# Performance work log

Measured on AMD Instinct MI355X. Metric: run time of the kernel, lower is better.

## Reference

```python
import jax, jax.numpy as jnp
import numpy as np

B, D, R, E, L = 16384, 1024, 64, 4, 3  # batch, in_features, low_rank, expert_num, layer_num


def setup_inputs() -> dict:
    key = jax.random.key(0)
    k0, k1, k2, k3, k4 = jax.random.split(key, 5)
    x = jax.random.normal(k0, (B, D), dtype=jnp.float32)
    # xavier_normal-ish init scales
    su = (2.0 / (D + R)) ** 0.5
    sc = (2.0 / (R + R)) ** 0.5
    U = jax.random.normal(k1, (L, E, D, R), dtype=jnp.float32) * su
    V = jax.random.normal(k2, (L, E, R, D), dtype=jnp.float32) * su
    C = jax.random.normal(k3, (L, E, R, R), dtype=jnp.float32) * sc
    bias = jnp.zeros((L, D), dtype=jnp.float32)  # original (L, D, 1) squeezed
    gates_w = jax.random.normal(k4, (E, D), dtype=jnp.float32) * (1.0 / D ** 0.5)
    return {"x": x, "U": U, "V": V, "C": C, "bias": bias, "gates_w": gates_w}


def reference(x, U, V, C, bias, gates_w):
    x0 = x                                  # [B, D]
    xl = x
    n_layers = U.shape[0]
    for i in range(n_layers):               # small fixed layer count
        g = jax.nn.softmax(xl @ gates_w.T, axis=1)          # [B, E] softmax over experts
        t = jnp.tanh(jnp.einsum('erd,bd->ber', V[i], xl))   # [B, E, R]
        t = jnp.tanh(jnp.einsum('ers,bes->ber', C[i], t))   # [B, E, R]
        t = jnp.einsum('edr,ber->bed', U[i], t) + bias[i][None, None, :]  # [B, E, D]
        t = x0[:, None, :] * t                               # x0 * E_i(xl)
        xl = jnp.einsum('bed,be->bd', t, g) + xl             # gated combine + residual
    return xl
```

## Files before the change

kernel.cpp:

```cpp
#include <hip/hip_runtime.h>
#include <hip/hip_bf16.h>


using bf16x8 = __attribute__((ext_vector_type(8))) short;
using f32x4  = __attribute__((ext_vector_type(4))) float;

__device__ __forceinline__ unsigned short f2bf(float f) {
  union { __hip_bfloat16 h; unsigned short s; } u;
  u.h = __float2bfloat16(f);
  return u.s;
}
__device__ __forceinline__ unsigned int pk2(float a, float b) {
  return (unsigned int)f2bf(a) | ((unsigned int)f2bf(b) << 16);
}
__device__ __forceinline__ float fast_tanh(float x) {
  float cx = fminf(15.0f, fmaxf(-15.0f, x));
  float t = exp2f(cx * 2.885390081777927f);
  return (t - 1.0f) / (t + 1.0f);
}

__global__ void preconvert_k(const float* __restrict__ U, const float* __restrict__ V,
                             const float* __restrict__ C, const float* __restrict__ G,
                             unsigned short* __restrict__ Vb, unsigned short* __restrict__ Ub,
                             unsigned short* __restrict__ Cb, unsigned short* __restrict__ Gb) {
  int i = blockIdx.x * 256 + threadIdx.x;
  if (i < 786432) { Vb[i] = f2bf(V[i]); Ub[i] = f2bf(U[i]); }
  if (i < 49152)  Cb[i] = f2bf(C[i]);
  if (i < 4096)   Gb[i] = f2bf(G[i]);
}

__global__ __launch_bounds__(512, 2)
void crossmix_layer(const float* xl_in, float* xl_out, const float* x0,
                    const unsigned short* __restrict__ Vb,
                    const unsigned short* __restrict__ Ub,
                    const unsigned short* __restrict__ Cb,
                    const unsigned short* __restrict__ Gb,
                    const float* __restrict__ bias) {
  constexpr int BM = 64, DD = 1024, BK = 128;
  __shared__ unsigned short xlbuf[2][BM * BK];
  __shared__ unsigned short tbuf[BM * 256];
  __shared__ float g_lds[BM][4];

  const int tid  = threadIdx.x;
  const int lane = tid & 63;
  const int wave = tid >> 6;
  const int l15  = lane & 15;
  const int l4   = lane >> 4;
  const int rowbase = blockIdx.x * BM;

  float4 sv[4];
  auto stage_load = [&](int c) {
    int r = tid >> 3, cb = (tid & 7) * 16;
    const float* s = xl_in + (size_t)(rowbase + r) * DD + c * BK + cb;
    sv[0] = *(const float4*)(s);
    sv[1] = *(const float4*)(s + 4);
    sv[2] = *(const float4*)(s + 8);
    sv[3] = *(const float4*)(s + 12);
  };
  auto stage_write = [&](int buf) {
    int r = tid >> 3, cb = (tid & 7) * 16;
    uint4 p0 = make_uint4(pk2(sv[0].x, sv[0].y), pk2(sv[0].z, sv[0].w),
                          pk2(sv[1].x, sv[1].y), pk2(sv[1].z, sv[1].w));
    uint4 p1 = make_uint4(pk2(sv[2].x, sv[2].y), pk2(sv[2].z, sv[2].w),
                          pk2(sv[3].x, sv[3].y), pk2(sv[3].z, sv[3].w));
    char* lb = (char*)xlbuf[buf];
    int base = r * 256 + cb * 2;
    int swz  = (r & 7) << 4;
    *(uint4*)(lb + ((base)      ^ swz)) = p0;
    *(uint4*)(lb + ((base + 16) ^ swz)) = p1;
  };

  f32x4 zf = {0.f, 0.f, 0.f, 0.f};
  f32x4 acc1[4][2], accg[4];
  #pragma unroll
  for (int m = 0; m < 4; ++m) { acc1[m][0] = zf; acc1[m][1] = zf; accg[m] = zf; }
  const int ncol = wave * 32;

  stage_load(0); stage_write(0);
  __syncthreads();
  for (int c = 0; c < 8; ++c) {
    if (c < 7) stage_load(c + 1);
    const char* lb = (const char*)xlbuf[c & 1];
    #pragma unroll
    for (int ki = 0; ki < 4; ++ki) {
      bf16x8 afr[4];
      #pragma unroll
      for (int mt = 0; mt < 4; ++mt) {
        int row = mt * 16 + l15;
        afr[mt] = *(const bf16x8*)(lb + ((row * 256 + ki * 64 + l4 * 16) ^ ((row & 7) << 4)));
      }
      int kg = c * 128 + ki * 32 + l4 * 8;
      #pragma unroll
      for (int nt = 0; nt < 2; ++nt) {
        bf16x8 bfr = *(const bf16x8*)(Vb + (ncol + nt * 16 + l15) * 1024 + kg);
        #pragma unroll
        for (int mt = 0; mt < 4; ++mt)
          acc1[mt][nt] = __builtin_amdgcn_mfma_f32_16x16x32_bf16(afr[mt], bfr, acc1[mt][nt], 0, 0, 0);
      }
      if (wave == 0) {
        bf16x8 gfr = {0, 0, 0, 0, 0, 0, 0, 0};
        if (l15 < 4) gfr = *(const bf16x8*)(Gb + l15 * 1024 + kg);
        #pragma unroll
        for (int mt = 0; mt < 4; ++mt)
          accg[mt] = __builtin_amdgcn_mfma_f32_16x16x32_bf16(afr[mt], gfr, accg[mt], 0, 0, 0);
      }
    }
    if (c < 7) stage_write((c + 1) & 1);
    __syncthreads();
  }

  if (wave == 0 && l15 < 4) {
    #pragma unroll
    for (int mt = 0; mt < 4; ++mt)
      #pragma unroll
      for (int rg = 0; rg < 4; ++rg)
        g_lds[mt * 16 + l4 * 4 + rg][l15] = accg[mt][rg];
  }
  #pragma unroll
  for (int mt = 0; mt < 4; ++mt)
    #pragma unroll
    for (int nt = 0; nt < 2; ++nt) {
      int col = ncol + nt * 16 + l15;
      #pragma unroll
      for (int rg = 0; rg < 4; ++rg) {
        int row = mt * 16 + l4 * 4 + rg;
        *(unsigned short*)((char*)tbuf + ((row * 512 + col * 2) ^ ((row & 7) << 4)))
            = f2bf(fast_tanh(acc1[mt][nt][rg]));
      }
    }
  __syncthreads();

  if (tid < BM) {
    float a0 = g_lds[tid][0], a1 = g_lds[tid][1], a2 = g_lds[tid][2], a3 = g_lds[tid][3];
    float mx = fmaxf(fmaxf(a0, a1), fmaxf(a2, a3));
    float e0 = exp2f((a0 - mx) * 1.442695041f);
    float e1 = exp2f((a1 - mx) * 1.442695041f);
    float e2 = exp2f((a2 - mx) * 1.442695041f);
    float e3 = exp2f((a3 - mx) * 1.442695041f);
    float inv = 1.0f / (e0 + e1 + e2 + e3);
    g_lds[tid][0] = e0 * inv; g_lds[tid][1] = e1 * inv;
    g_lds[tid][2] = e2 * inv; g_lds[tid][3] = e3 * inv;
  }
  __syncthreads();

  const int ex  = wave >> 1;
  const int cb2 = (wave & 1) * 32;
  f32x4 acc2[4][2];
  #pragma unroll
  for (int m = 0; m < 4; ++m) { acc2[m][0] = zf; acc2[m][1] = zf; }
  #pragma unroll
  for (int ki = 0; ki < 2; ++ki) {
    bf16x8 afr[4];
    #pragma unroll
    for (int mt = 0; mt < 4; ++mt) {
      int row = mt * 16 + l15;
      int kcol = ex * 64 + ki * 32 + l4 * 8;
      afr[mt] = *(const bf16x8*)((const char*)tbuf + ((row * 512 + kcol * 2) ^ ((row & 7) << 4)));
    }
    #pragma unroll
    for (int nt = 0; nt < 2; ++nt) {
      int rr = cb2 + nt * 16 + l15;
      bf16x8 bfr = *(const bf16x8*)(Cb + ex * 4096 + rr * 64 + ki * 32 + l4 * 8);
      #pragma unroll
      for (int mt = 0; mt < 4; ++mt)
        acc2[mt][nt] = __builtin_amdgcn_mfma_f32_16x16x32_bf16(afr[mt], bfr, acc2[mt][nt], 0, 0, 0);
    }
  }
  __syncthreads();
  #pragma unroll
  for (int mt = 0; mt < 4; ++mt)
    #pragma unroll
    for (int nt = 0; nt < 2; ++nt) {
      int col = ex * 64 + cb2 + nt * 16 + l15;
      #pragma unroll
      for (int rg = 0; rg < 4; ++rg) {
        int row = mt * 16 + l4 * 4 + rg;
        float gv = g_lds[row][ex];
        *(unsigned short*)((char*)tbuf + ((row * 512 + col * 2) ^ ((row & 7) << 4)))
            = f2bf(gv * fast_tanh(acc2[mt][nt][rg]));
      }
    }
  __syncthreads();

  #pragma unroll 1
  for (int ph = 0; ph < 2; ++ph) {
    f32x4 acc3[4][4];
    #pragma unroll
    for (int m = 0; m < 4; ++m)
      #pragma unroll
      for (int n = 0; n < 4; ++n) acc3[m][n] = zf;
    #pragma unroll 2
    for (int ki = 0; ki < 8; ++ki) {
      bf16x8 afr[4];
      #pragma unroll
      for (int mt = 0; mt < 4; ++mt) {
        int row = mt * 16 + l15;
        afr[mt] = *(const bf16x8*)((const char*)tbuf +
                   ((row * 512 + (ki * 32 + l4 * 8) * 2) ^ ((row & 7) << 4)));
      }
      int k = ki * 32 + l4 * 8;
      int ee = k >> 6, rr = k & 63;
      #pragma unroll
      for (int nt = 0; nt < 4; ++nt) {
        int d = ph * 512 + wave * 64 + nt * 16 + l15;
        bf16x8 bfr = *(const bf16x8*)(Ub + ee * 65536 + d * 64 + rr);
        #pragma unroll
        for (int mt = 0; mt < 4; ++mt)
          acc3[mt][nt] = __builtin_amdgcn_mfma_f32_16x16x32_bf16(afr[mt], bfr, acc3[mt][nt], 0, 0, 0);
      }
    }
    #pragma unroll
    for (int nt = 0; nt < 4; ++nt) {
      int d = ph * 512 + wave * 64 + nt * 16 + l15;
      float bv = bias[d];
      #pragma unroll
      for (int mt = 0; mt < 4; ++mt)
        #pragma unroll
        for (int rg = 0; rg < 4; ++rg) {
          size_t idx = (size_t)(rowbase + mt * 16 + l4 * 4 + rg) * DD + d;
          xl_out[idx] = xl_in[idx] + x0[idx] * (bv + acc3[mt][nt][rg]);
        }
    }
  }
}

extern "C" void kernel_launch(void* const* d_in, const int* in_sizes, int n_in,
                              void* d_out, int out_size, void* d_ws, size_t ws_size,
                              hipStream_t stream) {
  const float* x    = (const float*)d_in[0];
  const float* U    = (const float*)d_in[1];
  const float* V    = (const float*)d_in[2];
  const float* C    = (const float*)d_in[3];
  const float* bias = (const float*)d_in[4];
  const float* gw   = (const float*)d_in[5];
  float* out = (float*)d_out;

  unsigned short* Vb = (unsigned short*)d_ws;
  unsigned short* Ub = Vb + 786432;
  unsigned short* Cb = Ub + 786432;
  unsigned short* Gb = Cb + 49152;

  preconvert_k<<<dim3(3072), dim3(256), 0, stream>>>(U, V, C, gw, Vb, Ub, Cb, Gb);

  for (int l = 0; l < 3; ++l) {
    const float* xin = (l == 0) ? x : out;
    crossmix_layer<<<dim3(256), dim3(512), 0, stream>>>(
        xin, out, x,
        Vb + l * 262144, Ub + l * 262144, Cb + l * 16384, Gb,
        bias + l * 1024);
  }
}
```

Measured before the change: 395.1 us.

## Shrink row tile to 16 with 4-wave blocks and vectorize weight preconversion

The layer kernel now processes 16 rows per block with 256 threads instead of 64 rows with 512 threads, launching 1024 blocks instead of 256 so more blocks fill the GPU. Each wave now covers a wider slice of output columns, and the two-phase U stage becomes a single pass with 16 accumulators per wave. The cost is weight reuse: every block rereads the full V and U bf16 matrices for only 16 rows, so global and L2 traffic for weights rises roughly fourfold. The preconversion kernel is also vectorized to float4 loads and ushort4 stores.

```diff
diff --git a/kernel.cpp b/kernel.cpp
--- a/kernel.cpp
+++ b/kernel.cpp
@@ -19,24 +19,39 @@
   return (t - 1.0f) / (t + 1.0f);
 }
 
-__global__ void preconvert_k(const float* __restrict__ U, const float* __restrict__ V,
-                             const float* __restrict__ C, const float* __restrict__ G,
-                             unsigned short* __restrict__ Vb, unsigned short* __restrict__ Ub,
-                             unsigned short* __restrict__ Cb, unsigned short* __restrict__ Gb) {
+__global__ void preconvert_k(const float4* __restrict__ V4, const float4* __restrict__ U4,
+                             const float4* __restrict__ C4, const float4* __restrict__ G4,
+                             ushort4* __restrict__ Vb4, ushort4* __restrict__ Ub4,
+                             ushort4* __restrict__ Cb4, ushort4* __restrict__ Gb4) {
   int i = blockIdx.x * 256 + threadIdx.x;
-  if (i < 786432) { Vb[i] = f2bf(V[i]); Ub[i] = f2bf(U[i]); }
-  if (i < 49152)  Cb[i] = f2bf(C[i]);
-  if (i < 4096)   Gb[i] = f2bf(G[i]);
-}
-
-__global__ __launch_bounds__(512, 2)
-void crossmix_layer(const float* xl_in, float* xl_out, const float* x0,
+  if (i < 196608) {
+    float4 v = V4[i], u = U4[i];
+    ushort4 ov, ou;
+    ov.x = f2bf(v.x); ov.y = f2bf(v.y); ov.z = f2bf(v.z); ov.w = f2bf(v.w);
+    ou.x = f2bf(u.x); ou.y = f2bf(u.y); ou.z = f2bf(u.z); ou.w = f2bf(u.w);
+    Vb4[i] = ov; Ub4[i] = ou;
+  }
+  if (i < 12288) {
+    float4 c = C4[i];
+    ushort4 oc; oc.x = f2bf(c.x); oc.y = f2bf(c.y); oc.z = f2bf(c.z); oc.w = f2bf(c.w);
+    Cb4[i] = oc;
+  }
+  if (i < 1024) {
+    float4 g = G4[i];
+    ushort4 og; og.x = f2bf(g.x); og.y = f2bf(g.y); og.z = f2bf(g.z); og.w = f2bf(g.w);
+    Gb4[i] = og;
+  }
+}
+
+__global__ __launch_bounds__(256, 4)
+void crossmix_layer(const float* __restrict__ xl_in, float* __restrict__ xl_out,
+                    const float* __restrict__ x0,
                     const unsigned short* __restrict__ Vb,
                     const unsigned short* __restrict__ Ub,
                     const unsigned short* __restrict__ Cb,
                     const unsigned short* __restrict__ Gb,
                     const float* __restrict__ bias) {
-  constexpr int BM = 64, DD = 1024, BK = 128;
+  constexpr int BM = 16, DD = 1024, BK = 128;
   __shared__ unsigned short xlbuf[2][BM * BK];
   __shared__ unsigned short tbuf[BM * 256];
   __shared__ float g_lds[BM][4];
@@ -48,33 +63,27 @@
   const int l4   = lane >> 4;
   const int rowbase = blockIdx.x * BM;
 
-  float4 sv[4];
+  float4 sv[2];
   auto stage_load = [&](int c) {
-    int r = tid >> 3, cb = (tid & 7) * 16;
+    int r = tid >> 4, cb = (tid & 15) * 8;
     const float* s = xl_in + (size_t)(rowbase + r) * DD + c * BK + cb;
     sv[0] = *(const float4*)(s);
     sv[1] = *(const float4*)(s + 4);
-    sv[2] = *(const float4*)(s + 8);
-    sv[3] = *(const float4*)(s + 12);
   };
   auto stage_write = [&](int buf) {
-    int r = tid >> 3, cb = (tid & 7) * 16;
-    uint4 p0 = make_uint4(pk2(sv[0].x, sv[0].y), pk2(sv[0].z, sv[0].w),
-                          pk2(sv[1].x, sv[1].y), pk2(sv[1].z, sv[1].w));
-    uint4 p1 = make_uint4(pk2(sv[2].x, sv[2].y), pk2(sv[2].z, sv[2].w),
-                          pk2(sv[3].x, sv[3].y), pk2(sv[3].z, sv[3].w));
+    int r = tid >> 4, cb = (tid & 15) * 8;
+    uint4 p = make_uint4(pk2(sv[0].x, sv[0].y), pk2(sv[0].z, sv[0].w),
+                         pk2(sv[1].x, sv[1].y), pk2(sv[1].z, sv[1].w));
     char* lb = (char*)xlbuf[buf];
-    int base = r * 256 + cb * 2;
-    int swz  = (r & 7) << 4;
-    *(uint4*)(lb + ((base)      ^ swz)) = p0;
-    *(uint4*)(lb + ((base + 16) ^ swz)) = p1;
+    *(uint4*)(lb + ((r * 256 + cb * 2) ^ ((r & 7) << 4))) = p;
   };
 
   f32x4 zf = {0.f, 0.f, 0.f, 0.f};
-  f32x4 acc1[4][2], accg[4];
-  #pragma unroll
-  for (int m = 0; m < 4; ++m) { acc1[m][0] = zf; acc1[m][1] = zf; accg[m] = zf; }
-  const int ncol = wave * 32;
+  f32x4 acc1[4], accg;
+  #pragma unroll
+  for (int n = 0; n < 4; ++n) acc1[n] = zf;
+  accg = zf;
+  const int ncol = wave * 64;
 
   stage_load(0); stage_write(0);
   __syncthreads();
@@ -83,26 +92,17 @@
     const char* lb = (const char*)xlbuf[c & 1];
     #pragma unroll
     for (int ki = 0; ki < 4; ++ki) {
-      bf16x8 afr[4];
-      #pragma unroll
-      for (int mt = 0; mt < 4; ++mt) {
-        int row = mt * 16 + l15;
-        afr[mt] = *(const bf16x8*)(lb + ((row * 256 + ki * 64 + l4 * 16) ^ ((row & 7) << 4)));
-      }
+      bf16x8 afr = *(const bf16x8*)(lb + ((l15 * 256 + ki * 64 + l4 * 16) ^ ((l15 & 7) << 4)));
       int kg = c * 128 + ki * 32 + l4 * 8;
       #pragma unroll
-      for (int nt = 0; nt < 2; ++nt) {
+      for (int nt = 0; nt < 4; ++nt) {
         bf16x8 bfr = *(const bf16x8*)(Vb + (ncol + nt * 16 + l15) * 1024 + kg);
-        #pragma unroll
-        for (int mt = 0; mt < 4; ++mt)
-          acc1[mt][nt] = __builtin_amdgcn_mfma_f32_16x16x32_bf16(afr[mt], bfr, acc1[mt][nt], 0, 0, 0);
+        acc1[nt] = __builtin_amdgcn_mfma_f32_16x16x32_bf16(afr, bfr, acc1[nt], 0, 0, 0);
       }
       if (wave == 0) {
         bf16x8 gfr = {0, 0, 0, 0, 0, 0, 0, 0};
         if (l15 < 4) gfr = *(const bf16x8*)(Gb + l15 * 1024 + kg);
-        #pragma unroll
-        for (int mt = 0; mt < 4; ++mt)
-          accg[mt] = __builtin_amdgcn_mfma_f32_16x16x32_bf16(afr[mt], gfr, accg[mt], 0, 0, 0);
+        accg = __builtin_amdgcn_mfma_f32_16x16x32_bf16(afr, gfr, accg, 0, 0, 0);
       }
     }
     if (c < 7) stage_write((c + 1) & 1);
@@ -111,23 +111,19 @@
 
   if (wave == 0 && l15 < 4) {
     #pragma unroll
-    for (int mt = 0; mt < 4; ++mt)
-      #pragma unroll
-      for (int rg = 0; rg < 4; ++rg)
-        g_lds[mt * 16 + l4 * 4 + rg][l15] = accg[mt][rg];
-  }
-  #pragma unroll
-  for (int mt = 0; mt < 4; ++mt)
-    #pragma unroll
-    for (int nt = 0; nt < 2; ++nt) {
-      int col = ncol + nt * 16 + l15;
-      #pragma unroll
-      for (int rg = 0; rg < 4; ++rg) {
-        int row = mt * 16 + l4 * 4 + rg;
-        *(unsigned short*)((char*)tbuf + ((row * 512 + col * 2) ^ ((row & 7) << 4)))
-            = f2bf(fast_tanh(acc1[mt][nt][rg]));
-      }
-    }
+    for (int rg = 0; rg < 4; ++rg)
+      g_lds[l4 * 4 + rg][l15] = accg[rg];
+  }
+  #pragma unroll
+  for (int nt = 0; nt < 4; ++nt) {
+    int col = ncol + nt * 16 + l15;
+    #pragma unroll
+    for (int rg = 0; rg < 4; ++rg) {
+      int row = l4 * 4 + rg;
+      *(unsigned short*)((char*)tbuf + ((row * 512 + col * 2) ^ ((row & 7) << 4)))
+          = f2bf(fast_tanh(acc1[nt][rg]));
+    }
+  }
   __syncthreads();
 
   if (tid < BM) {
@@ -143,83 +139,57 @@
   }
   __syncthreads();
 
-  const int ex  = wave >> 1;
-  const int cb2 = (wave & 1) * 32;
-  f32x4 acc2[4][2];
-  #pragma unroll
-  for (int m = 0; m < 4; ++m) { acc2[m][0] = zf; acc2[m][1] = zf; }
+  const int ex = wave;
+  f32x4 acc2[4];
+  #pragma unroll
+  for (int n = 0; n < 4; ++n) acc2[n] = zf;
   #pragma unroll
   for (int ki = 0; ki < 2; ++ki) {
-    bf16x8 afr[4];
-    #pragma unroll
-    for (int mt = 0; mt < 4; ++mt) {
-      int row = mt * 16 + l15;
-      int kcol = ex * 64 + ki * 32 + l4 * 8;
-      afr[mt] = *(const bf16x8*)((const char*)tbuf + ((row * 512 + kcol * 2) ^ ((row & 7) << 4)));
-    }
-    #pragma unroll
-    for (int nt = 0; nt < 2; ++nt) {
-      int rr = cb2 + nt * 16 + l15;
-      bf16x8 bfr = *(const bf16x8*)(Cb + ex * 4096 + rr * 64 + ki * 32 + l4 * 8);
-      #pragma unroll
-      for (int mt = 0; mt < 4; ++mt)
-        acc2[mt][nt] = __builtin_amdgcn_mfma_f32_16x16x32_bf16(afr[mt], bfr, acc2[mt][nt], 0, 0, 0);
-    }
-  }
-  __syncthreads();
-  #pragma unroll
-  for (int mt = 0; mt < 4; ++mt)
-    #pragma unroll
-    for (int nt = 0; nt < 2; ++nt) {
-      int col = ex * 64 + cb2 + nt * 16 + l15;
-      #pragma unroll
-      for (int rg = 0; rg < 4; ++rg) {
-        int row = mt * 16 + l4 * 4 + rg;
-        float gv = g_lds[row][ex];
-        *(unsigned short*)((char*)tbuf + ((row * 512 + col * 2) ^ ((row & 7) << 4)))
-            = f2bf(gv * fast_tanh(acc2[mt][nt][rg]));
-      }
-    }
-  __syncthreads();
-
-  #pragma unroll 1
-  for (int ph = 0; ph < 2; ++ph) {
-    f32x4 acc3[4][4];
-    #pragma unroll
-    for (int m = 0; m < 4; ++m)
-      #pragma unroll
-      for (int n = 0; n < 4; ++n) acc3[m][n] = zf;
-    #pragma unroll 2
-    for (int ki = 0; ki < 8; ++ki) {
-      bf16x8 afr[4];
-      #pragma unroll
-      for (int mt = 0; mt < 4; ++mt) {
-        int row = mt * 16 + l15;
-        afr[mt] = *(const bf16x8*)((const char*)tbuf +
-                   ((row * 512 + (ki * 32 + l4 * 8) * 2) ^ ((row & 7) << 4)));
-      }
-      int k = ki * 32 + l4 * 8;
-      int ee = k >> 6, rr = k & 63;
-      #pragma unroll
-      for (int nt = 0; nt < 4; ++nt) {
-        int d = ph * 512 + wave * 64 + nt * 16 + l15;
-        bf16x8 bfr = *(const bf16x8*)(Ub + ee * 65536 + d * 64 + rr);
-        #pragma unroll
-        for (int mt = 0; mt < 4; ++mt)
-          acc3[mt][nt] = __builtin_amdgcn_mfma_f32_16x16x32_bf16(afr[mt], bfr, acc3[mt][nt], 0, 0, 0);
-      }
-    }
+    int kcol = ex * 64 + ki * 32 + l4 * 8;
+    bf16x8 afr = *(const bf16x8*)((const char*)tbuf + ((l15 * 512 + kcol * 2) ^ ((l15 & 7) << 4)));
     #pragma unroll
     for (int nt = 0; nt < 4; ++nt) {
-      int d = ph * 512 + wave * 64 + nt * 16 + l15;
-      float bv = bias[d];
-      #pragma unroll
-      for (int mt = 0; mt < 4; ++mt)
-        #pragma unroll
-        for (int rg = 0; rg < 4; ++rg) {
-          size_t idx = (size_t)(rowbase + mt * 16 + l4 * 4 + rg) * DD + d;
-          xl_out[idx] = xl_in[idx] + x0[idx] * (bv + acc3[mt][nt][rg]);
-        }
+      bf16x8 bfr = *(const bf16x8*)(Cb + ex * 4096 + (nt * 16 + l15) * 64 + ki * 32 + l4 * 8);
+      acc2[nt] = __builtin_amdgcn_mfma_f32_16x16x32_bf16(afr, bfr, acc2[nt], 0, 0, 0);
+    }
+  }
+  __syncthreads();
+  #pragma unroll
+  for (int nt = 0; nt < 4; ++nt) {
+    int col = ex * 64 + nt * 16 + l15;
+    #pragma unroll
+    for (int rg = 0; rg < 4; ++rg) {
+      int row = l4 * 4 + rg;
+      float gv = g_lds[row][ex];
+      *(unsigned short*)((char*)tbuf + ((row * 512 + col * 2) ^ ((row & 7) << 4)))
+          = f2bf(gv * fast_tanh(acc2[nt][rg]));
+    }
+  }
+  __syncthreads();
+
+  f32x4 acc3[16];
+  #pragma unroll
+  for (int n = 0; n < 16; ++n) acc3[n] = zf;
+  #pragma unroll 2
+  for (int ki = 0; ki < 8; ++ki) {
+    int kcol = ki * 32 + l4 * 8;
+    bf16x8 afr = *(const bf16x8*)((const char*)tbuf + ((l15 * 512 + kcol * 2) ^ ((l15 & 7) << 4)));
+    int ee = kcol >> 6, rr = kcol & 63;
+    #pragma unroll
+    for (int nt = 0; nt < 16; ++nt) {
+      int d = wave * 256 + nt * 16 + l15;
+      bf16x8 bfr = *(const bf16x8*)(Ub + ee * 65536 + d * 64 + rr);
+      acc3[nt] = __builtin_amdgcn_mfma_f32_16x16x32_bf16(afr, bfr, acc3[nt], 0, 0, 0);
+    }
+  }
+  #pragma unroll
+  for (int nt = 0; nt < 16; ++nt) {
+    int d = wave * 256 + nt * 16 + l15;
+    float bv = bias[d];
+    #pragma unroll
+    for (int rg = 0; rg < 4; ++rg) {
+      size_t idx = (size_t)(rowbase + l4 * 4 + rg) * DD + d;
+      xl_out[idx] = xl_in[idx] + x0[idx] * (bv + acc3[nt][rg]);
     }
   }
 }
@@ -240,11 +210,13 @@
   unsigned short* Cb = Ub + 786432;
   unsigned short* Gb = Cb + 49152;
 
-  preconvert_k<<<dim3(3072), dim3(256), 0, stream>>>(U, V, C, gw, Vb, Ub, Cb, Gb);
+  preconvert_k<<<dim3(768), dim3(256), 0, stream>>>(
+      (const float4*)V, (const float4*)U, (const float4*)C, (const float4*)gw,
+      (ushort4*)Vb, (ushort4*)Ub, (ushort4*)Cb, (ushort4*)Gb);
 
   for (int l = 0; l < 3; ++l) {
     const float* xin = (l == 0) ? x : out;
-    crossmix_layer<<<dim3(256), dim3(512), 0, stream>>>(
+    crossmix_layer<<<dim3(1024), dim3(256), 0, stream>>>(
         xin, out, x,
         Vb + l * 262144, Ub + l * 262144, Cb + l * 16384, Gb,
         bias + l * 1024);
```

Result: slower. 547.3 us (+38.5%).
